# Performance work log

Measured on AMD Instinct MI355X. Metric: run time of the kernel, lower is better.

The kernel has to match this reference:

```python
import jax, jax.numpy as jnp
import numpy as np

B, L, HSIZE = 16, 512, 1024
H, D = 16, 64  # HHEAD = HSIZE/base, HBASE = 64

def setup_inputs() -> dict:
    key = jax.random.key(0)
    ks = jax.random.split(key, 10)
    inp = {
        'v': jax.random.normal(ks[0], (B, L, HSIZE), jnp.float32),
        'k': jax.random.normal(ks[1], (B, L, HSIZE), jnp.float32),
        'q': jax.random.normal(ks[2], (B, L, HSIZE), jnp.float32),
        'img_abs': jax.random.normal(ks[3], (B, L, HSIZE), jnp.float32),
        'Wv': jax.random.normal(ks[4], (HSIZE, HSIZE), jnp.float32) * 0.02,
        'Wk': jax.random.normal(ks[5], (HSIZE, HSIZE), jnp.float32) * 0.02,
        'Wq': jax.random.normal(ks[6], (HSIZE, HSIZE), jnp.float32) * 0.02,
        'Wm': jax.random.normal(ks[7], (HSIZE, HSIZE), jnp.float32) * 0.02,
        'abs_mask': jax.random.bernoulli(ks[8], 0.1, (B, 1, L, L)),
        'mask': jax.random.bernoulli(ks[9], 0.1, (B, 1, L, L)),
    }
    return inp

def reference(v, k, q, img_abs, Wv, Wk, Wq, Wm, abs_mask, mask):
    nb = q.shape[0]
    # Linear (no bias) then split heads: [B, L, HSIZE] -> [B, H, L, D]
    def heads(x):
        return x.reshape(nb, -1, H, D).transpose(0, 2, 1, 3)
    vh = heads(v @ Wv.T)
    kh = heads(k @ Wk.T)
    qh = heads(q @ Wq.T)
    ph = heads(img_abs)
    scale = 1.0 / jnp.sqrt(jnp.asarray(D, qh.dtype))
    # modulate: attention of q over positional features, residual-added to q
    s1 = jnp.einsum('bhqd,bhpd->bhqp', qh, ph) * scale
    s1 = jnp.where(abs_mask, jnp.asarray(-1e9, s1.dtype), s1)
    qh = qh + jnp.einsum('bhqp,bhpd->bhqd', jax.nn.softmax(s1, axis=-1), ph)
    # main attention (dropout = identity in eval mode)
    s2 = jnp.einsum('bhqd,bhkd->bhqk', qh, kh) * scale
    s2 = jnp.where(mask, jnp.asarray(-1e9, s2.dtype), s2)
    atted = jnp.einsum('bhqk,bhkd->bhqd', jax.nn.softmax(s2, axis=-1), vh)
    atted = atted.transpose(0, 2, 1, 3).reshape(nb, -1, H * D)
    return atted @ Wm.T
```

## Files before the change

### kernel.cpp

```cpp
#include <hip/hip_runtime.h>

typedef unsigned short u16;
typedef unsigned int u32;
typedef unsigned long long u64;
typedef __attribute__((ext_vector_type(8))) short short8;
typedef __attribute__((ext_vector_type(4))) float f32x4;

#define NB 16
#define SL 512
#define HS 1024
#define NHEAD 16
#define HD 64
#define NTOKC (16L * 512 * 1024)
#define NWC   (1024L * 1024)
#define NMC   (16L * 512 * 512)

typedef const __attribute__((address_space(1))) u32* gas_t;
typedef __attribute__((address_space(3))) u32* las_t;

__device__ __forceinline__ void gld16(const u16* g, u16* l) {
  __builtin_amdgcn_global_load_lds((gas_t)g, (las_t)l, 16, 0, 0);
}

__device__ __forceinline__ u16 f2bf(float f) {
  union { float f; unsigned u; } c; c.f = f;
  unsigned r = c.u + 0x7FFFu + ((c.u >> 16) & 1u);
  return (u16)(r >> 16);
}
__device__ __forceinline__ float bf2f(u16 u) {
  union { float f; unsigned u; } c; c.u = ((unsigned)u) << 16;
  return c.f;
}

__global__ __launch_bounds__(256) void prep(
    const float* __restrict__ v, const float* __restrict__ k,
    const float* __restrict__ q, const float* __restrict__ img,
    const float* __restrict__ Wv, const float* __restrict__ Wk,
    const float* __restrict__ Wq, const float* __restrict__ Wm,
    const int* __restrict__ absm, const int* __restrict__ mask,
    u16* __restrict__ ovk, u16* __restrict__ xq, u16* __restrict__ pb,
    u16* __restrict__ w4, u64* __restrict__ bits) {
  const int y = blockIdx.y;
  const long bx = blockIdx.x;
  if (y < 4) {
    const float* in = y == 0 ? v : y == 1 ? k : y == 2 ? q : img;
    u16* out = y == 0 ? ovk : y == 1 ? ovk + NTOKC : y == 2 ? xq : pb;
    long i = (bx * 256 + threadIdx.x) * 4;
    float4 f = *(const float4*)(in + i);
    uint2 u;
    u.x = (unsigned)f2bf(f.x) | ((unsigned)f2bf(f.y) << 16);
    u.y = (unsigned)f2bf(f.z) | ((unsigned)f2bf(f.w) << 16);
    *(uint2*)(out + i) = u;
  } else if (y == 4) {
    if (bx >= 4096) return;
    long i = bx * 1024 + threadIdx.x * 4;
    int j = (int)(i >> 20);
    const float* in = j == 0 ? Wv : j == 1 ? Wk : j == 2 ? Wq : Wm;
    long off = i & (NWC - 1);
    float4 f = *(const float4*)(in + off);
    uint2 u;
    u.x = (unsigned)f2bf(f.x) | ((unsigned)f2bf(f.y) << 16);
    u.y = (unsigned)f2bf(f.z) | ((unsigned)f2bf(f.w) << 16);
    *(uint2*)(w4 + i) = u;
  } else {
#pragma unroll
    for (int rep = 0; rep < 4; ++rep) {
      long i = (bx * 4 + rep) * 256 + threadIdx.x;
      const int* m = (i >= NMC) ? mask : absm;
      long off = i & (NMC - 1);
      u64 bset = __ballot(m[off] != 0);
      if ((threadIdx.x & 63) == 0) bits[i >> 6] = bset;
    }
  }
}

__global__ __launch_bounds__(256) void gemm_p3(const u16* __restrict__ Avk,
                                               const u16* __restrict__ Aq,
                                               const u16* __restrict__ W4,
                                               u16* __restrict__ Cb) {
  __shared__ u16 As[128 * 64];
  __shared__ u16 Bs[128 * 64];
  const int tid = threadIdx.x;
  const int wave = tid >> 6, lane = tid & 63;
  const int quad = lane >> 4, l16 = lane & 15;
  const int l7 = l16 & 7;
  const int sel = blockIdx.x >> 6;
  const int row0 = (blockIdx.x & 63) * 128, col0 = blockIdx.y * 128;
  const int wm = (wave >> 1) * 64, wn = (wave & 1) * 64;
  const int lrow = lane >> 3;
  const int scb = (lane & 7) ^ lrow;
  const int K = HS, N = HS;

  const u16* A = (sel == 2) ? Aq : Avk + (long)sel * NTOKC;
  const u16* W = W4 + (long)sel * NWC;
  u16* C = Cb + (long)sel * NTOKC;

  f32x4 acc[4][4];
#pragma unroll
  for (int mt = 0; mt < 4; ++mt)
#pragma unroll
    for (int nt = 0; nt < 4; ++nt) acc[mt][nt] = (f32x4){0.f, 0.f, 0.f, 0.f};

  const u16* Ab = A + (long)row0 * K;
  const u16* Wb = W + (long)col0 * K;

  for (int k0 = 0; k0 < K; k0 += 64) {
    __syncthreads();
#pragma unroll
    for (int it = 0; it < 4; ++it) {
      int seg = wave * 4 + it;
      int r = seg * 8 + lrow;
      gld16(Ab + (long)r * K + k0 + scb * 8, As + seg * 512);
      gld16(Wb + (long)r * K + k0 + scb * 8, Bs + seg * 512);
    }
    __syncthreads();
#pragma unroll
    for (int kt = 0; kt < 2; ++kt) {
      short8 af[4], bw[4];
#pragma unroll
      for (int mt = 0; mt < 4; ++mt)
        af[mt] = *(const short8*)(As + (wm + mt * 16 + l16) * 64 +
                                  (((kt * 4 + quad) ^ l7) * 8));
#pragma unroll
      for (int nt = 0; nt < 4; ++nt)
        bw[nt] = *(const short8*)(Bs + (wn + nt * 16 + l16) * 64 +
                                  (((kt * 4 + quad) ^ l7) * 8));
#pragma unroll
      for (int mt = 0; mt < 4; ++mt)
#pragma unroll
        for (int nt = 0; nt < 4; ++nt)
          acc[mt][nt] = __builtin_amdgcn_mfma_f32_16x16x32_bf16(
              af[mt], bw[nt], acc[mt][nt], 0, 0, 0);
    }
  }
#pragma unroll
  for (int mt = 0; mt < 4; ++mt)
#pragma unroll
    for (int nt = 0; nt < 4; ++nt)
#pragma unroll
      for (int i = 0; i < 4; ++i) {
        long r = row0 + wm + mt * 16 + quad * 4 + i;
        long c = col0 + wn + nt * 16 + l16;
        C[r * N + c] = f2bf(acc[mt][nt][i]);
      }
}

__global__ __launch_bounds__(256) void gemm_f(const u16* __restrict__ A,
                                              const u16* __restrict__ W,
                                              float* __restrict__ C) {
  __shared__ u16 As[128 * 64];
  __shared__ u16 Bs[128 * 64];
  const int tid = threadIdx.x;
  const int wave = tid >> 6, lane = tid & 63;
  const int quad = lane >> 4, l16 = lane & 15;
  const int l7 = l16 & 7;
  const int row0 = blockIdx.x * 128, col0 = blockIdx.y * 128;
  const int wm = (wave >> 1) * 64, wn = (wave & 1) * 64;
  const int lrow = lane >> 3;
  const int scb = (lane & 7) ^ lrow;
  const int K = HS, N = HS;

  f32x4 acc[4][4];
#pragma unroll
  for (int mt = 0; mt < 4; ++mt)
#pragma unroll
    for (int nt = 0; nt < 4; ++nt) acc[mt][nt] = (f32x4){0.f, 0.f, 0.f, 0.f};

  const u16* Ab = A + (long)row0 * K;
  const u16* Wb = W + (long)col0 * K;

  for (int k0 = 0; k0 < K; k0 += 64) {
    __syncthreads();
#pragma unroll
    for (int it = 0; it < 4; ++it) {
      int seg = wave * 4 + it;
      int r = seg * 8 + lrow;
      gld16(Ab + (long)r * K + k0 + scb * 8, As + seg * 512);
      gld16(Wb + (long)r * K + k0 + scb * 8, Bs + seg * 512);
    }
    __syncthreads();
#pragma unroll
    for (int kt = 0; kt < 2; ++kt) {
      short8 af[4], bw[4];
#pragma unroll
      for (int mt = 0; mt < 4; ++mt)
        af[mt] = *(const short8*)(As + (wm + mt * 16 + l16) * 64 +
                                  (((kt * 4 + quad) ^ l7) * 8));
#pragma unroll
      for (int nt = 0; nt < 4; ++nt)
        bw[nt] = *(const short8*)(Bs + (wn + nt * 16 + l16) * 64 +
                                  (((kt * 4 + quad) ^ l7) * 8));
#pragma unroll
      for (int mt = 0; mt < 4; ++mt)
#pragma unroll
        for (int nt = 0; nt < 4; ++nt)
          acc[mt][nt] = __builtin_amdgcn_mfma_f32_16x16x32_bf16(
              af[mt], bw[nt], acc[mt][nt], 0, 0, 0);
    }
  }
#pragma unroll
  for (int mt = 0; mt < 4; ++mt)
#pragma unroll
    for (int nt = 0; nt < 4; ++nt)
#pragma unroll
      for (int i = 0; i < 4; ++i) {
        long r = row0 + wm + mt * 16 + quad * 4 + i;
        long c = col0 + wn + nt * 16 + l16;
        C[r * N + c] = acc[mt][nt][i];
      }
}

template <bool SAME>
__device__ __forceinline__ void attn_stage(
    const u16* __restrict__ Kb, const u16* __restrict__ Vb,
    const u32* __restrict__ Mb, int q0, short8 qf[2], float l_i[4],
    f32x4 o[4], u16 (*Ks)[72], u16 (*Vs)[72], u16 (*Ps)[76],
    int wave, int quad, int l16, int sr, int sds, int vcol) {
  uint4 kp = *(const uint4*)(Kb + (long)sr * HS + sds);
  uint4 vp = SAME ? kp : *(const uint4*)(Vb + (long)sr * HS + sds);
  for (int t = 0; t < 8; ++t) {
    __syncthreads();
    *(uint4*)&Ks[sr][sds] = kp;
    {
      union { uint4 q; u16 e[8]; } tv;
      tv.q = SAME ? kp : vp;
#pragma unroll
      for (int j = 0; j < 8; ++j) Vs[sds + j][vcol] = tv.e[j];
    }
    __syncthreads();
    if (t < 7) {
      kp = *(const uint4*)(Kb + (long)((t + 1) * 64 + sr) * HS + sds);
      if (!SAME)
        vp = *(const uint4*)(Vb + (long)((t + 1) * 64 + sr) * HS + sds);
    }
    f32x4 s[4];
#pragma unroll
    for (int nt = 0; nt < 4; ++nt) s[nt] = (f32x4){0.f, 0.f, 0.f, 0.f};
#pragma unroll
    for (int kt = 0; kt < 2; ++kt)
#pragma unroll
      for (int nt = 0; nt < 4; ++nt) {
        short8 bk = *(const short8*)&Ks[nt * 16 + l16][kt * 32 + quad * 8];
        s[nt] = __builtin_amdgcn_mfma_f32_16x16x32_bf16(qf[kt], bk, s[nt], 0, 0, 0);
      }
#pragma unroll
    for (int i = 0; i < 4; ++i) {
      int gr = q0 + wave * 16 + quad * 4 + i;
      uint2 mw = *(const uint2*)&Mb[(long)gr * 16 + t * 2];
#pragma unroll
      for (int nt = 0; nt < 4; ++nt) {
        u32 w = (nt & 2) ? mw.y : mw.x;
        int msk = (w >> ((nt & 1) * 16 + l16)) & 1;
        float p = msk ? 0.f : __expf(s[nt][i] * 0.125f);
        l_i[i] += p;
        Ps[wave * 16 + quad * 4 + i][nt * 16 + l16] = f2bf(p);
      }
    }
#pragma unroll
    for (int kt = 0; kt < 2; ++kt) {
      short8 ap = *(const short8*)&Ps[wave * 16 + l16][kt * 32 + quad * 8];
#pragma unroll
      for (int nt = 0; nt < 4; ++nt) {
        short8 bv = *(const short8*)&Vs[nt * 16 + l16]
                                      [(kt * 32 + quad * 8) ^ ((nt & 3) << 4)];
        o[nt] = __builtin_amdgcn_mfma_f32_16x16x32_bf16(ap, bv, o[nt], 0, 0, 0);
      }
    }
  }
}

__global__ __launch_bounds__(512, 4) void attn_fused(
    const u16* __restrict__ Qp, const u16* __restrict__ Pbp,
    const u16* __restrict__ Kp, const u16* __restrict__ Vp,
    const u32* __restrict__ B0, const u32* __restrict__ B1,
    u16* __restrict__ Op) {
  __shared__ u16 Ks[64][72];
  __shared__ u16 Vs[64][72];
  __shared__ u16 Ps[128][76];
  const int tid = threadIdx.x;
  const int wave = tid >> 6, lane = tid & 63;
  const int quad = lane >> 4, l16 = lane & 15;
  const int qt = blockIdx.x, h = blockIdx.y, b = blockIdx.z;
  const int q0 = qt * 128;
  const long bs = (long)SL * HS;
  const u16* Qb = Qp + (long)b * bs + h * HD;
  const u16* Pb = Pbp + (long)b * bs + h * HD;
  const u16* Kb = Kp + (long)b * bs + h * HD;
  const u16* Vb = Vp + (long)b * bs + h * HD;
  const u32* M0 = B0 + (long)b * SL * 16;
  const u32* M1 = B1 + (long)b * SL * 16;
  const int sr = tid >> 3, sds = (tid & 7) * 8;
  const int vcol = sr ^ (((sds >> 4) & 3) << 4);

  short8 qf[2];
#pragma unroll
  for (int kt = 0; kt < 2; ++kt)
    qf[kt] = *(const short8*)(Qb + (long)(q0 + wave * 16 + l16) * HS +
                              kt * 32 + quad * 8);

  float l_i[4] = {0.f, 0.f, 0.f, 0.f};
  f32x4 o[4];
#pragma unroll
  for (int nt = 0; nt < 4; ++nt) o[nt] = (f32x4){0.f, 0.f, 0.f, 0.f};

  attn_stage<true>(Pb, Pb, M0, q0, qf, l_i, o, Ks, Vs, Ps, wave, quad, l16,
                   sr, sds, vcol);

#pragma unroll
  for (int i = 0; i < 4; ++i) {
    float rs = l_i[i];
#pragma unroll
    for (int off = 8; off >= 1; off >>= 1) rs += __shfl_xor(rs, off, 64);
    float inv = 1.f / rs;
#pragma unroll
    for (int nt = 0; nt < 4; ++nt)
      Ps[wave * 16 + quad * 4 + i][nt * 16 + l16] = f2bf(o[nt][i] * inv);
    l_i[i] = 0.f;
  }
#pragma unroll
  for (int kt = 0; kt < 2; ++kt) {
    short8 t8 = *(const short8*)&Ps[wave * 16 + l16][kt * 32 + quad * 8];
#pragma unroll
    for (int j = 0; j < 8; ++j)
      qf[kt][j] = (short)f2bf(bf2f((u16)t8[j]) + bf2f((u16)qf[kt][j]));
  }
#pragma unroll
  for (int nt = 0; nt < 4; ++nt) o[nt] = (f32x4){0.f, 0.f, 0.f, 0.f};

  attn_stage<false>(Kb, Vb, M1, q0, qf, l_i, o, Ks, Vs, Ps, wave, quad, l16,
                    sr, sds, vcol);

  u16* Ob = Op + (long)b * bs + h * HD;
#pragma unroll
  for (int i = 0; i < 4; ++i) {
    float rs = l_i[i];
#pragma unroll
    for (int off = 8; off >= 1; off >>= 1) rs += __shfl_xor(rs, off, 64);
    float inv = 1.f / rs;
    int r = q0 + wave * 16 + quad * 4 + i;
#pragma unroll
    for (int nt = 0; nt < 4; ++nt)
      Ob[(long)r * HS + nt * 16 + l16] = f2bf(o[nt][i] * inv);
  }
}

extern "C" void kernel_launch(void* const* d_in, const int* in_sizes, int n_in,
                              void* d_out, int out_size, void* d_ws,
                              size_t ws_size, hipStream_t stream) {
  const float* v   = (const float*)d_in[0];
  const float* k   = (const float*)d_in[1];
  const float* q   = (const float*)d_in[2];
  const float* img = (const float*)d_in[3];
  const float* Wv  = (const float*)d_in[4];
  const float* Wk  = (const float*)d_in[5];
  const float* Wq  = (const float*)d_in[6];
  const float* Wm  = (const float*)d_in[7];
  const int* absm  = (const int*)d_in[8];
  const int* mask  = (const int*)d_in[9];
  float* out = (float*)d_out;

  const long NTOK = NTOKC;
  const long NW   = NWC;
  const long NM   = NMC;
  u16* ovk = (u16*)d_out;
  u16* ws  = (u16*)d_ws;
  u16* xq  = ws;
  u16* pb  = ws + 1 * NTOK;
  u16* vh  = ws + 2 * NTOK;
  u16* kh  = ws + 3 * NTOK;
  u16* qh  = ws + 4 * NTOK;
  u16* w4  = ws + 5 * NTOK;
  u64* bt0 = (u64*)(w4 + 4 * NW);
  u64* bt1 = bt0 + NM / 64;
  u16* att = xq;

  prep<<<dim3(8192, 6), 256, 0, stream>>>(v, k, q, img, Wv, Wk, Wq, Wm,
                                          absm, mask, ovk, xq, pb, w4, bt0);
  gemm_p3<<<dim3(192, 8), 256, 0, stream>>>(ovk, xq, w4, vh);
  attn_fused<<<dim3(SL / 128, NHEAD, NB), 512, 0, stream>>>(
      qh, pb, kh, vh, (const u32*)bt0, (const u32*)bt1, att);
  gemm_f<<<dim3(NB * SL / 128, HS / 128), 256, 0, stream>>>(att, w4 + 3 * NW,
                                                            out);
}
```

Measured before the change: 388.1 us.

## Compute transposed S^T tiles and pass P via cross-lane shuffles instead of LDS

The QK^T MFMA now computes S transposed (K tile as the A operand), so each lane holds the scores for one query row and loads a single 64-bit mask word per tile. The probabilities are packed into bf16 pairs in registers and rearranged into the PV A-operand layout with __shfl, which removes the Ps shared-memory buffer and its write/read round trip. LDS shrinks to one combined K/V array, which is reused for the residual q update. In exchange each tile adds 16 shuffles, and register pressure may rise.

```diff
diff --git a/kernel.cpp b/kernel.cpp
--- a/kernel.cpp
+++ b/kernel.cpp
@@ -5,6 +5,7 @@
 typedef unsigned long long u64;
 typedef __attribute__((ext_vector_type(8))) short short8;
 typedef __attribute__((ext_vector_type(4))) float f32x4;
+typedef __attribute__((ext_vector_type(4))) u32 u32x4;
 
 #define NB 16
 #define SL 512
@@ -213,11 +214,12 @@
 template <bool SAME>
 __device__ __forceinline__ void attn_stage(
     const u16* __restrict__ Kb, const u16* __restrict__ Vb,
-    const u32* __restrict__ Mb, int q0, short8 qf[2], float l_i[4],
-    f32x4 o[4], u16 (*Ks)[72], u16 (*Vs)[72], u16 (*Ps)[76],
-    int wave, int quad, int l16, int sr, int sds, int vcol) {
+    const u64* __restrict__ Mb, int qrow, short8 qf[2], float& l_p,
+    f32x4 o[4], u16 (*Ks)[72], u16 (*Vs)[72],
+    int quad, int l16, int sr, int sds, int vcol) {
   uint4 kp = *(const uint4*)(Kb + (long)sr * HS + sds);
-  uint4 vp = SAME ? kp : *(const uint4*)(Vb + (long)sr * HS + sds);
+  uint4 vp;
+  if (!SAME) vp = *(const uint4*)(Vb + (long)sr * HS + sds);
   for (int t = 0; t < 8; ++t) {
     __syncthreads();
     *(uint4*)&Ks[sr][sds] = kp;
@@ -233,6 +235,7 @@
       if (!SAME)
         vp = *(const uint4*)(Vb + (long)((t + 1) * 64 + sr) * HS + sds);
     }
+    const u64 mw = Mb[(long)qrow * 8 + t];
     f32x4 s[4];
 #pragma unroll
     for (int nt = 0; nt < 4; ++nt) s[nt] = (f32x4){0.f, 0.f, 0.f, 0.f};
@@ -240,30 +243,45 @@
     for (int kt = 0; kt < 2; ++kt)
 #pragma unroll
       for (int nt = 0; nt < 4; ++nt) {
-        short8 bk = *(const short8*)&Ks[nt * 16 + l16][kt * 32 + quad * 8];
-        s[nt] = __builtin_amdgcn_mfma_f32_16x16x32_bf16(qf[kt], bk, s[nt], 0, 0, 0);
-      }
-#pragma unroll
-    for (int i = 0; i < 4; ++i) {
-      int gr = q0 + wave * 16 + quad * 4 + i;
-      uint2 mw = *(const uint2*)&Mb[(long)gr * 16 + t * 2];
-#pragma unroll
-      for (int nt = 0; nt < 4; ++nt) {
-        u32 w = (nt & 2) ? mw.y : mw.x;
-        int msk = (w >> ((nt & 1) * 16 + l16)) & 1;
-        float p = msk ? 0.f : __expf(s[nt][i] * 0.125f);
-        l_i[i] += p;
-        Ps[wave * 16 + quad * 4 + i][nt * 16 + l16] = f2bf(p);
-      }
-    }
+        short8 ak = *(const short8*)&Ks[nt * 16 + l16][kt * 32 + quad * 8];
+        s[nt] = __builtin_amdgcn_mfma_f32_16x16x32_bf16(ak, qf[kt], s[nt],
+                                                        0, 0, 0);
+      }
+    u32 pk[8];
+    float lp = 0.f;
+#pragma unroll
+    for (int nt = 0; nt < 4; ++nt) {
+      const u32 mb = (u32)(mw >> (nt * 16 + quad * 4));
+#pragma unroll
+      for (int ih = 0; ih < 2; ++ih) {
+        float p0 = (mb & (1u << (2 * ih))) ? 0.f
+                                           : __expf(s[nt][2 * ih] * 0.125f);
+        float p1 = (mb & (1u << (2 * ih + 1)))
+                       ? 0.f
+                       : __expf(s[nt][2 * ih + 1] * 0.125f);
+        lp += p0 + p1;
+        pk[nt * 2 + ih] = (u32)f2bf(p0) | ((u32)f2bf(p1) << 16);
+      }
+    }
+    l_p += lp;
 #pragma unroll
     for (int kt = 0; kt < 2; ++kt) {
-      short8 ap = *(const short8*)&Ps[wave * 16 + l16][kt * 32 + quad * 8];
+      u32x4 av;
+#pragma unroll
+      for (int j2 = 0; j2 < 4; ++j2) {
+        int src = ((quad & 1) * 2 + (j2 >> 1)) * 16 + l16;
+        u32 vlo = (u32)__shfl((int)pk[(2 * kt) * 2 + (j2 & 1)], src, 64);
+        u32 vhi = (u32)__shfl((int)pk[(2 * kt + 1) * 2 + (j2 & 1)], src, 64);
+        av[j2] = (quad & 2) ? vhi : vlo;
+      }
+      union { u32x4 u; short8 s8; } cv;
+      cv.u = av;
 #pragma unroll
       for (int nt = 0; nt < 4; ++nt) {
         short8 bv = *(const short8*)&Vs[nt * 16 + l16]
                                       [(kt * 32 + quad * 8) ^ ((nt & 3) << 4)];
-        o[nt] = __builtin_amdgcn_mfma_f32_16x16x32_bf16(ap, bv, o[nt], 0, 0, 0);
+        o[nt] = __builtin_amdgcn_mfma_f32_16x16x32_bf16(cv.s8, bv, o[nt],
+                                                        0, 0, 0);
       }
     }
   }
@@ -272,11 +290,11 @@
 __global__ __launch_bounds__(512, 4) void attn_fused(
     const u16* __restrict__ Qp, const u16* __restrict__ Pbp,
     const u16* __restrict__ Kp, const u16* __restrict__ Vp,
-    const u32* __restrict__ B0, const u32* __restrict__ B1,
+    const u64* __restrict__ B0, const u64* __restrict__ B1,
     u16* __restrict__ Op) {
-  __shared__ u16 Ks[64][72];
-  __shared__ u16 Vs[64][72];
-  __shared__ u16 Ps[128][76];
+  __shared__ u16 KV[128][72];
+  u16 (*Ks)[72] = KV;
+  u16 (*Vs)[72] = KV + 64;
   const int tid = threadIdx.x;
   const int wave = tid >> 6, lane = tid & 63;
   const int quad = lane >> 4, l16 = lane & 15;
@@ -287,60 +305,71 @@
   const u16* Pb = Pbp + (long)b * bs + h * HD;
   const u16* Kb = Kp + (long)b * bs + h * HD;
   const u16* Vb = Vp + (long)b * bs + h * HD;
-  const u32* M0 = B0 + (long)b * SL * 16;
-  const u32* M1 = B1 + (long)b * SL * 16;
+  const u64* M0 = B0 + (long)b * SL * 8;
+  const u64* M1 = B1 + (long)b * SL * 8;
   const int sr = tid >> 3, sds = (tid & 7) * 8;
   const int vcol = sr ^ (((sds >> 4) & 3) << 4);
+  const int qrow = q0 + wave * 16 + l16;
 
   short8 qf[2];
 #pragma unroll
   for (int kt = 0; kt < 2; ++kt)
-    qf[kt] = *(const short8*)(Qb + (long)(q0 + wave * 16 + l16) * HS +
-                              kt * 32 + quad * 8);
-
-  float l_i[4] = {0.f, 0.f, 0.f, 0.f};
+    qf[kt] = *(const short8*)(Qb + (long)qrow * HS + kt * 32 + quad * 8);
+
+  float l_p = 0.f;
   f32x4 o[4];
 #pragma unroll
   for (int nt = 0; nt < 4; ++nt) o[nt] = (f32x4){0.f, 0.f, 0.f, 0.f};
 
-  attn_stage<true>(Pb, Pb, M0, q0, qf, l_i, o, Ks, Vs, Ps, wave, quad, l16,
-                   sr, sds, vcol);
-
-#pragma unroll
-  for (int i = 0; i < 4; ++i) {
-    float rs = l_i[i];
-#pragma unroll
-    for (int off = 8; off >= 1; off >>= 1) rs += __shfl_xor(rs, off, 64);
+  attn_stage<true>(Pb, Pb, M0, qrow, qf, l_p, o, Ks, Vs, quad, l16, sr, sds,
+                   vcol);
+
+  {
+    float rs = l_p;
+    rs += __shfl_xor(rs, 16, 64);
+    rs += __shfl_xor(rs, 32, 64);
     float inv = 1.f / rs;
-#pragma unroll
-    for (int nt = 0; nt < 4; ++nt)
-      Ps[wave * 16 + quad * 4 + i][nt * 16 + l16] = f2bf(o[nt][i] * inv);
-    l_i[i] = 0.f;
-  }
-#pragma unroll
-  for (int kt = 0; kt < 2; ++kt) {
-    short8 t8 = *(const short8*)&Ps[wave * 16 + l16][kt * 32 + quad * 8];
-#pragma unroll
-    for (int j = 0; j < 8; ++j)
-      qf[kt][j] = (short)f2bf(bf2f((u16)t8[j]) + bf2f((u16)qf[kt][j]));
-  }
-#pragma unroll
-  for (int nt = 0; nt < 4; ++nt) o[nt] = (f32x4){0.f, 0.f, 0.f, 0.f};
-
-  attn_stage<false>(Kb, Vb, M1, q0, qf, l_i, o, Ks, Vs, Ps, wave, quad, l16,
-                    sr, sds, vcol);
-
-  u16* Ob = Op + (long)b * bs + h * HD;
-#pragma unroll
-  for (int i = 0; i < 4; ++i) {
-    float rs = l_i[i];
-#pragma unroll
-    for (int off = 8; off >= 1; off >>= 1) rs += __shfl_xor(rs, off, 64);
+    float invq[4];
+#pragma unroll
+    for (int i = 0; i < 4; ++i) invq[i] = __shfl(inv, quad * 4 + i, 64);
+    __syncthreads();
+#pragma unroll
+    for (int i = 0; i < 4; ++i)
+#pragma unroll
+      for (int nt = 0; nt < 4; ++nt)
+        KV[wave * 16 + quad * 4 + i][nt * 16 + l16] =
+            f2bf(o[nt][i] * invq[i]);
+#pragma unroll
+    for (int kt = 0; kt < 2; ++kt) {
+      short8 t8 = *(const short8*)&KV[wave * 16 + l16][kt * 32 + quad * 8];
+#pragma unroll
+      for (int j = 0; j < 8; ++j)
+        qf[kt][j] = (short)f2bf(bf2f((u16)t8[j]) + bf2f((u16)qf[kt][j]));
+    }
+#pragma unroll
+    for (int nt = 0; nt < 4; ++nt) o[nt] = (f32x4){0.f, 0.f, 0.f, 0.f};
+    l_p = 0.f;
+  }
+
+  attn_stage<false>(Kb, Vb, M1, qrow, qf, l_p, o, Ks, Vs, quad, l16, sr, sds,
+                    vcol);
+
+  {
+    float rs = l_p;
+    rs += __shfl_xor(rs, 16, 64);
+    rs += __shfl_xor(rs, 32, 64);
     float inv = 1.f / rs;
-    int r = q0 + wave * 16 + quad * 4 + i;
-#pragma unroll
-    for (int nt = 0; nt < 4; ++nt)
-      Ob[(long)r * HS + nt * 16 + l16] = f2bf(o[nt][i] * inv);
+    float invq[4];
+#pragma unroll
+    for (int i = 0; i < 4; ++i) invq[i] = __shfl(inv, quad * 4 + i, 64);
+    u16* Ob = Op + (long)b * bs + h * HD;
+#pragma unroll
+    for (int i = 0; i < 4; ++i) {
+      int r = q0 + wave * 16 + quad * 4 + i;
+#pragma unroll
+      for (int nt = 0; nt < 4; ++nt)
+        Ob[(long)r * HS + nt * 16 + l16] = f2bf(o[nt][i] * invq[i]);
+    }
   }
 }
 
@@ -378,7 +407,7 @@
                                           absm, mask, ovk, xq, pb, w4, bt0);
   gemm_p3<<<dim3(192, 8), 256, 0, stream>>>(ovk, xq, w4, vh);
   attn_fused<<<dim3(SL / 128, NHEAD, NB), 512, 0, stream>>>(
-      qh, pb, kh, vh, (const u32*)bt0, (const u32*)bt1, att);
+      qh, pb, kh, vh, bt0, bt1, att);
   gemm_f<<<dim3(NB * SL / 128, HS / 128), 256, 0, stream>>>(att, w4 + 3 * NW,
                                                             out);
 }
```

After: 383.3 us. Within noise of the previous version (-1.2%).
